# Performance work log

Measured on AMD Instinct MI355X. Metric: run time of the kernel, lower is better.

## Reference

```python
import jax, jax.numpy as jnp
import numpy as np

N_NODES = 100000
N_EDGES = 1600000
DIM = 64
NEG_SLOPE = 0.2  # DGL GATConv default
BN_EPS = 1e-5


def setup_inputs() -> dict:
    key = jax.random.key(0)
    ks = jax.random.split(key, 16)
    d = {}
    d["node_weight"] = jax.random.normal(ks[0], (N_NODES, DIM), jnp.float32)
    d["edge_weight"] = jax.random.normal(ks[1], (N_EDGES,), jnp.float32)  # unused in forward (faithful to source)
    d["src"] = jax.random.randint(ks[2], (N_EDGES,), 0, N_NODES)
    d["dst"] = jax.random.randint(ks[3], (N_EDGES,), 0, N_NODES)
    i = 4
    scale = 1.0 / np.sqrt(DIM)
    for l in (1, 2, 3):
        d[f"W{l}"] = jax.random.normal(ks[i], (DIM, DIM), jnp.float32) * scale; i += 1
        d[f"al{l}"] = jax.random.normal(ks[i], (DIM,), jnp.float32) * 0.1; i += 1
        d[f"ar{l}"] = jax.random.normal(ks[i], (DIM,), jnp.float32) * 0.1; i += 1
        d[f"b{l}"] = jnp.zeros((DIM,), jnp.float32)
        d[f"g{l}"] = jnp.ones((DIM,), jnp.float32)
        d[f"beta{l}"] = jnp.zeros((DIM,), jnp.float32)
    return d


def gat_layer(h, src, dst, W, al, ar, b):
    # DGL GATConv, 1 head: project, edge attention, per-dst softmax, scatter-add
    feat = h @ W                                  # [N, D]
    el = feat @ al                                # [N]
    er = feat @ ar                                # [N]
    e = jax.nn.leaky_relu(el[src] + er[dst], NEG_SLOPE)   # [E]
    m = jax.ops.segment_max(e, dst, num_segments=N_NODES)  # per-dst max
    ex = jnp.exp(e - m[dst])
    s = jax.ops.segment_sum(ex, dst, num_segments=N_NODES)
    alpha = ex / s[dst]                           # edge softmax
    out = jax.ops.segment_sum(alpha[:, None] * feat[src], dst, num_segments=N_NODES)
    return out + b


def batchnorm(h, g, beta):
    # BatchNorm1d in training mode: batch stats, biased variance
    mu = jnp.mean(h, axis=0)
    var = jnp.mean(jnp.square(h - mu), axis=0)
    return (h - mu) * jax.lax.rsqrt(var + BN_EPS) * g + beta


def reference(node_weight, edge_weight, src, dst,
              W1, al1, ar1, b1, g1, beta1,
              W2, al2, ar2, b2, g2, beta2,
              W3, al3, ar3, b3, g3, beta3):
    # dropout is identity in eval mode
    h = gat_layer(node_weight, src, dst, W1, al1, ar1, b1)
    h = jax.nn.elu(batchnorm(h, g1, beta1))
    h = gat_layer(h, src, dst, W2, al2, ar2, b2)
    h = jax.nn.elu(batchnorm(h, g2, beta2))
    h = gat_layer(h, src, dst, W3, al3, ar3, b3)
    h = batchnorm(h, g3, beta3)
    return h
```

## Files before the change

### kernel.cpp

```cpp
#include <hip/hip_runtime.h>
#include <hip/hip_bf16.h>
#include <math.h>

#define DIM 64
#define BSHIFT 9
#define BNODES 512
#define MAXB 256
#define EPT 8
#define CHUNK 2048

typedef __attribute__((ext_vector_type(8))) short bf16x8;
typedef __attribute__((ext_vector_type(4))) float f32x4;

__device__ __forceinline__ short f2bf(float x) {
    union { __hip_bfloat16 b; short s; } u;
    u.b = __float2bfloat16(x);
    return u.s;
}
__device__ __forceinline__ float bf2f(short s) {
    return __uint_as_float(((unsigned)(unsigned short)s) << 16);
}


__global__ void bin_count_kernel(const int* __restrict__ dst, int* __restrict__ bucket_cnt, int E) {
    __shared__ int h[MAXB];
    int t = threadIdx.x;
    h[t] = 0;
    __syncthreads();
    for (int i = blockIdx.x * blockDim.x + t; i < E; i += gridDim.x * blockDim.x)
        atomicAdd(&h[dst[i] >> BSHIFT], 1);
    __syncthreads();
    if (h[t]) atomicAdd(&bucket_cnt[t], h[t]);
}

__global__ void bucket_scan_kernel(const int* __restrict__ bucket_cnt,
                                   int* __restrict__ bucket_off, int* __restrict__ bucket_fill) {
    __shared__ int s[MAXB];
    int t = threadIdx.x;
    int v = bucket_cnt[t];
    s[t] = v;
    __syncthreads();
    for (int off = 1; off < MAXB; off <<= 1) {
        int x = (t >= off) ? s[t - off] : 0;
        __syncthreads();
        s[t] += x;
        __syncthreads();
    }
    bucket_off[t] = s[t] - v;
    bucket_fill[t] = 0;
}

__global__ __launch_bounds__(256) void bin_scatter_kernel(
    const int* __restrict__ src, const int* __restrict__ dst,
    const int* __restrict__ bucket_off, int* __restrict__ bucket_fill,
    unsigned long long* __restrict__ binned, int E) {
    __shared__ int lcnt[MAXB];
    __shared__ int lbase[MAXB];
    int t = threadIdx.x;
    lcnt[t] = 0;
    __syncthreads();
    int base = blockIdx.x * CHUNK;
    unsigned long long pair[EPT];
    int slot[EPT];
#pragma unroll
    for (int j = 0; j < EPT; j++) {
        int idx = base + j * 256 + t;
        if (idx < E) {
            int s = src[idx], d = dst[idx];
            pair[j] = ((unsigned long long)(unsigned)d << 32) | (unsigned)s;
            slot[j] = atomicAdd(&lcnt[d >> BSHIFT], 1);
        } else {
            slot[j] = -1;
        }
    }
    __syncthreads();
    int c = lcnt[t];
    if (c) lbase[t] = atomicAdd(&bucket_fill[t], c);
    __syncthreads();
#pragma unroll
    for (int j = 0; j < EPT; j++) {
        if (slot[j] >= 0) {
            int b = (int)(pair[j] >> 32) >> BSHIFT;
            binned[(size_t)bucket_off[b] + lbase[b] + slot[j]] = pair[j];
        }
    }
}

__global__ __launch_bounds__(256) void node_count_kernel(
    const unsigned long long* __restrict__ binned, const int* __restrict__ bucket_off,
    const int* __restrict__ bucket_cnt, int* __restrict__ counts, int N) {
    __shared__ int cnt[BNODES];
    int b = blockIdx.x, t = threadIdx.x;
    for (int i = t; i < BNODES; i += 256) cnt[i] = 0;
    __syncthreads();
    int s0 = bucket_off[b], c = bucket_cnt[b];
    for (int i = t; i < c; i += 256) {
        int d = (int)(binned[(size_t)s0 + i] >> 32);
        atomicAdd(&cnt[d & (BNODES - 1)], 1);
    }
    __syncthreads();
    int nbase = b << BSHIFT;
    for (int i = t; i < BNODES; i += 256)
        if (nbase + i < N) counts[nbase + i] = cnt[i];
}

__global__ void scan1_kernel(const int* __restrict__ counts, int* __restrict__ excl,
                             int* __restrict__ blk_sums, int n) {
    __shared__ int sdata[256];
    int t = threadIdx.x;
    int base = blockIdx.x * 1024 + t * 4;
    int v0 = (base + 0 < n) ? counts[base + 0] : 0;
    int v1 = (base + 1 < n) ? counts[base + 1] : 0;
    int v2 = (base + 2 < n) ? counts[base + 2] : 0;
    int v3 = (base + 3 < n) ? counts[base + 3] : 0;
    int tsum = v0 + v1 + v2 + v3;
    sdata[t] = tsum;
    __syncthreads();
    for (int off = 1; off < 256; off <<= 1) {
        int x = (t >= off) ? sdata[t - off] : 0;
        __syncthreads();
        sdata[t] += x;
        __syncthreads();
    }
    int run = sdata[t] - tsum;
    if (base + 0 < n) excl[base + 0] = run; run += v0;
    if (base + 1 < n) excl[base + 1] = run; run += v1;
    if (base + 2 < n) excl[base + 2] = run; run += v2;
    if (base + 3 < n) excl[base + 3] = run;
    if (t == 255) blk_sums[blockIdx.x] = sdata[255];
}

__global__ void scan2_kernel(int* __restrict__ blk_sums, int nb) {
    __shared__ int s[128];
    int t = threadIdx.x;
    s[t] = (t < nb) ? blk_sums[t] : 0;
    __syncthreads();
    for (int off = 1; off < 128; off <<= 1) {
        int x = (t >= off) ? s[t - off] : 0;
        __syncthreads();
        s[t] += x;
        __syncthreads();
    }
    if (t < nb) blk_sums[t] = (t > 0) ? s[t - 1] : 0;
}

__global__ void scan3_kernel(int* __restrict__ excl, const int* __restrict__ blk_sums,
                             int n, int total) {
    int i = blockIdx.x * blockDim.x + threadIdx.x;
    if (i < n) excl[i] += blk_sums[i >> 10];
    if (i == 0) excl[n] = total;
}

__global__ __launch_bounds__(256) void final_scatter_kernel(
    const unsigned long long* __restrict__ binned, const int* __restrict__ bucket_off,
    const int* __restrict__ bucket_cnt, const int* __restrict__ row_ptr,
    int* __restrict__ src_sorted, int N) {
    __shared__ int fill[BNODES];
    int b = blockIdx.x, t = threadIdx.x;
    for (int i = t; i < BNODES; i += 256) fill[i] = 0;
    __syncthreads();
    int s0 = bucket_off[b], c = bucket_cnt[b];
    for (int i = t; i < c; i += 256) {
        unsigned long long p = binned[(size_t)s0 + i];
        int d = (int)(p >> 32);
        int pos = row_ptr[d] + atomicAdd(&fill[d & (BNODES - 1)], 1);
        src_sorted[pos] = (int)(p & 0xffffffffu);
    }
}


__global__ __launch_bounds__(256) void gemm64_mfma_kernel(
    const float* __restrict__ h, const float* __restrict__ W,
    const float* __restrict__ al, const float* __restrict__ ar,
    const float* __restrict__ stats, const float* __restrict__ g,
    const float* __restrict__ beta, int do_bn, float invN,
    __hip_bfloat16* __restrict__ feat, float* __restrict__ el, float* __restrict__ er,
    int n) {
    int t = threadIdx.x;
    int lane = t & 63;
    int li = lane & 15;
    int quad = lane >> 4;
    int wv = t >> 6;

    bf16x8 b_hi[2][4], b_lo[2][4];
#pragma unroll
    for (int ks = 0; ks < 2; ks++)
#pragma unroll
        for (int nt = 0; nt < 4; nt++) {
#pragma unroll
            for (int j = 0; j < 8; j++) {
                float w = W[(ks * 32 + quad * 8 + j) * 64 + nt * 16 + li];
                short hi = f2bf(w);
                b_hi[ks][nt][j] = hi;
                b_lo[ks][nt][j] = f2bf(w - bf2f(hi));
            }
        }
    float alv[4], arv[4];
#pragma unroll
    for (int nt = 0; nt < 4; nt++) { alv[nt] = al[nt * 16 + li]; arv[nt] = ar[nt * 16 + li]; }

    float sc[2][8], sh[2][8];
    if (do_bn) {
#pragma unroll
        for (int ks = 0; ks < 2; ks++)
#pragma unroll
            for (int j = 0; j < 8; j++) {
                int k = ks * 32 + quad * 8 + j;
                float mu = stats[k] * invN;
                float var = fmaf(-mu, mu, stats[64 + k] * invN);
                float inv = rsqrtf(var + 1e-5f) * g[k];
                sc[ks][j] = inv;
                sh[ks][j] = beta[k] - mu * inv;
            }
    }

    int ntiles = (n + 15) >> 4;
    for (int tile = blockIdx.x * 4 + wv; tile < ntiles; tile += gridDim.x * 4) {
        int m0 = tile << 4;
        int rrow = m0 + li;
        const float* rowp = h + (size_t)((rrow < n) ? rrow : (n - 1)) * 64;
        bf16x8 a_hi[2], a_lo[2];
#pragma unroll
        for (int ks = 0; ks < 2; ks++) {
            float4 v0 = *(const float4*)(rowp + ks * 32 + quad * 8);
            float4 v1 = *(const float4*)(rowp + ks * 32 + quad * 8 + 4);
            float x[8] = {v0.x, v0.y, v0.z, v0.w, v1.x, v1.y, v1.z, v1.w};
#pragma unroll
            for (int j = 0; j < 8; j++) {
                float v = x[j];
                if (do_bn) {
                    v = fmaf(v, sc[ks][j], sh[ks][j]);
                    if (v < 0.f) v = expm1f(v);
                }
                short hi = f2bf(v);
                a_hi[ks][j] = hi;
                a_lo[ks][j] = f2bf(v - bf2f(hi));
            }
        }
        f32x4 acc[4];
#pragma unroll
        for (int nt = 0; nt < 4; nt++) acc[nt] = (f32x4){0.f, 0.f, 0.f, 0.f};
#pragma unroll
        for (int ks = 0; ks < 2; ks++)
#pragma unroll
            for (int nt = 0; nt < 4; nt++) {
                acc[nt] = __builtin_amdgcn_mfma_f32_16x16x32_bf16(a_hi[ks], b_hi[ks][nt], acc[nt], 0, 0, 0);
                acc[nt] = __builtin_amdgcn_mfma_f32_16x16x32_bf16(a_lo[ks], b_hi[ks][nt], acc[nt], 0, 0, 0);
                acc[nt] = __builtin_amdgcn_mfma_f32_16x16x32_bf16(a_hi[ks], b_lo[ks][nt], acc[nt], 0, 0, 0);
            }
#pragma unroll
        for (int nt = 0; nt < 4; nt++)
#pragma unroll
            for (int reg = 0; reg < 4; reg++) {
                int wrow = m0 + quad * 4 + reg;
                if (wrow < n) {
                    union { __hip_bfloat16 b; short s; } u;
                    u.s = f2bf(acc[nt][reg]);
                    feat[(size_t)wrow * 64 + nt * 16 + li] = u.b;
                }
            }
        float pl[4], pr[4];
#pragma unroll
        for (int reg = 0; reg < 4; reg++) {
            float l = 0.f, r = 0.f;
#pragma unroll
            for (int nt = 0; nt < 4; nt++) {
                l = fmaf(acc[nt][reg], alv[nt], l);
                r = fmaf(acc[nt][reg], arv[nt], r);
            }
#pragma unroll
            for (int off = 1; off < 16; off <<= 1) {
                l += __shfl_xor(l, off, 64);
                r += __shfl_xor(r, off, 64);
            }
            pl[reg] = l; pr[reg] = r;
        }
        int row = m0 + quad * 4;
        if (li == 0 && row < n)          { el[row] = pl[0]; er[row] = pr[0]; }
        else if (li == 1 && row + 1 < n) { el[row + 1] = pl[1]; er[row + 1] = pr[1]; }
        else if (li == 2 && row + 2 < n) { el[row + 2] = pl[2]; er[row + 2] = pr[2]; }
        else if (li == 3 && row + 3 < n) { el[row + 3] = pl[3]; er[row + 3] = pr[3]; }
    }
}

__global__ __launch_bounds__(256) void attn_agg_kernel(
    const int* __restrict__ row_ptr, const int* __restrict__ src_sorted,
    const float* __restrict__ el, const float* __restrict__ er,
    const __hip_bfloat16* __restrict__ feat, const float* __restrict__ bias,
    float* __restrict__ out, int n) {
    int t = threadIdx.x, lane = t & 63;
    int q = lane >> 3;
    int li = lane & 7;
    int node = blockIdx.x * 4 + (t >> 6);
    if (node >= n) return;
    int start = row_ptr[node], end = row_ptr[node + 1];
    float er_n = er[node];
    const uint4* featv = (const uint4*)feat;

    float s = 0.f;
    float a0 = 0.f, a1 = 0.f, a2 = 0.f, a3 = 0.f, a4 = 0.f, a5 = 0.f, a6 = 0.f, a7 = 0.f;

    int i = start;
    bool v0 = false;
    uint4 p0 = {0u, 0u, 0u, 0u};
    float el0 = 0.f;
    if (i < end) {
        int idx = i + q;
        v0 = idx < end;
        int idc = v0 ? idx : end - 1;
        int sn = src_sorted[idc];
        el0 = el[sn];
        p0 = featv[(size_t)sn * 8 + li];
    }
    while (i < end) {
        int inext = i + 8;
        bool v1 = false;
        uint4 p1 = {0u, 0u, 0u, 0u};
        float el1 = 0.f;
        if (inext < end) {
            int idx = inext + q;
            v1 = idx < end;
            int idc = v1 ? idx : end - 1;
            int sn = src_sorted[idc];
            el1 = el[sn];
            p1 = featv[(size_t)sn * 8 + li];
        }
        float e = el0 + er_n;
        e = (e > 0.f) ? e : 0.2f * e;
        float w = v0 ? __expf(e) : 0.f;
        s += w;
        a0 = fmaf(w, __uint_as_float(p0.x << 16), a0);
        a1 = fmaf(w, __uint_as_float(p0.x & 0xffff0000u), a1);
        a2 = fmaf(w, __uint_as_float(p0.y << 16), a2);
        a3 = fmaf(w, __uint_as_float(p0.y & 0xffff0000u), a3);
        a4 = fmaf(w, __uint_as_float(p0.z << 16), a4);
        a5 = fmaf(w, __uint_as_float(p0.z & 0xffff0000u), a5);
        a6 = fmaf(w, __uint_as_float(p0.w << 16), a6);
        a7 = fmaf(w, __uint_as_float(p0.w & 0xffff0000u), a7);
        i = inext; v0 = v1; p0 = p1; el0 = el1;
    }
#pragma unroll
    for (int off = 8; off <= 32; off <<= 1) {
        s  += __shfl_xor(s,  off, 64);
        a0 += __shfl_xor(a0, off, 64);
        a1 += __shfl_xor(a1, off, 64);
        a2 += __shfl_xor(a2, off, 64);
        a3 += __shfl_xor(a3, off, 64);
        a4 += __shfl_xor(a4, off, 64);
        a5 += __shfl_xor(a5, off, 64);
        a6 += __shfl_xor(a6, off, 64);
        a7 += __shfl_xor(a7, off, 64);
    }
    float inv_s = (s > 0.f) ? 1.f / s : 0.f;
    if (q == 0) {
        const float4* bv = (const float4*)bias;
        float4 b0 = bv[li * 2], b1 = bv[li * 2 + 1];
        float4 o0 = {fmaf(a0, inv_s, b0.x), fmaf(a1, inv_s, b0.y),
                     fmaf(a2, inv_s, b0.z), fmaf(a3, inv_s, b0.w)};
        float4 o1 = {fmaf(a4, inv_s, b1.x), fmaf(a5, inv_s, b1.y),
                     fmaf(a6, inv_s, b1.z), fmaf(a7, inv_s, b1.w)};
        float4* op = (float4*)(out + (size_t)node * 64 + li * 8);
        op[0] = o0;
        op[1] = o1;
    }
}

__global__ __launch_bounds__(256) void bn_stats_kernel(const float* __restrict__ h,
                                                       float* __restrict__ stats, int n) {
    __shared__ float ls[256], lss[256];
    int t = threadIdx.x, lane = t & 63;
    int w = blockIdx.x * 4 + (t >> 6);
    int stride = gridDim.x * 4;
    float s = 0.f, ss = 0.f;
    for (int row = w; row < n; row += stride) {
        float v = h[(size_t)row * DIM + lane];
        s += v;
        ss = fmaf(v, v, ss);
    }
    ls[t] = s; lss[t] = ss;
    __syncthreads();
    if (t < 64) {
        float a = ls[t] + ls[t + 64] + ls[t + 128] + ls[t + 192];
        float b = lss[t] + lss[t + 64] + lss[t + 128] + lss[t + 192];
        atomicAdd(&stats[t], a);
        atomicAdd(&stats[64 + t], b);
    }
}

__global__ void bn_apply_kernel(float* __restrict__ h, const float* __restrict__ stats,
                                const float* __restrict__ g, const float* __restrict__ beta,
                                int n, int do_elu) {
    int i = blockIdx.x * blockDim.x + threadIdx.x;
    int total = n * DIM;
    int stride = gridDim.x * blockDim.x;
    float invN = 1.f / (float)n;
    for (; i < total; i += stride) {
        int c = i & 63;
        float mu = stats[c] * invN;
        float var = fmaf(-mu, mu, stats[DIM + c] * invN);
        float x = (h[i] - mu) * rsqrtf(var + 1e-5f) * g[c] + beta[c];
        if (do_elu && x < 0.f) x = expm1f(x);
        h[i] = x;
    }
}


extern "C" void kernel_launch(void* const* d_in, const int* in_sizes, int n_in,
                              void* d_out, int out_size, void* d_ws, size_t ws_size,
                              hipStream_t stream) {
    const float* nw = (const float*)d_in[0];
    const int* src = (const int*)d_in[2];
    const int* dst = (const int*)d_in[3];
    const int N = in_sizes[0] / DIM;
    const int E = in_sizes[2];
    const float invN = 1.f / (float)N;
    const int nbuck = (N + BNODES - 1) >> BSHIFT;

    char* ws = (char*)d_ws;
    size_t off = 0;
    auto alloc = [&](size_t bytes) -> void* {
        void* p = ws + off;
        off += (bytes + 255) & ~(size_t)255;
        return p;
    };
    int* counts       = (int*)alloc((size_t)N * 4);
    int* row_ptr      = (int*)alloc(((size_t)N + 1) * 4);
    int* blk_sums     = (int*)alloc(512);
    int* bucket_cnt   = (int*)alloc(MAXB * 4);
    int* bucket_off   = (int*)alloc(MAXB * 4);
    int* bucket_fill  = (int*)alloc(MAXB * 4);
    unsigned long long* binned = (unsigned long long*)alloc((size_t)E * 8);
    int* src_sorted   = (int*)alloc((size_t)E * 4);
    float* el         = (float*)alloc((size_t)N * 4);
    float* er         = (float*)alloc((size_t)N * 4);
    __hip_bfloat16* feat = (__hip_bfloat16*)alloc((size_t)N * DIM * 2);
    float* hbuf       = (float*)alloc((size_t)N * DIM * 4);
    float* stats      = (float*)alloc(3 * 512);

    int nb = (N + 1023) / 1024;

    hipMemsetAsync(bucket_cnt, 0, MAXB * 4, stream);
    hipMemsetAsync(stats, 0, 3 * 512, stream);
    bin_count_kernel<<<256, 256, 0, stream>>>(dst, bucket_cnt, E);
    bucket_scan_kernel<<<1, MAXB, 0, stream>>>(bucket_cnt, bucket_off, bucket_fill);
    bin_scatter_kernel<<<(E + CHUNK - 1) / CHUNK, 256, 0, stream>>>(
        src, dst, bucket_off, bucket_fill, binned, E);
    node_count_kernel<<<nbuck, 256, 0, stream>>>(binned, bucket_off, bucket_cnt, counts, N);
    scan1_kernel<<<nb, 256, 0, stream>>>(counts, row_ptr, blk_sums, N);
    scan2_kernel<<<1, 128, 0, stream>>>(blk_sums, nb);
    scan3_kernel<<<(N + 255) / 256, 256, 0, stream>>>(row_ptr, blk_sums, N, E);
    final_scatter_kernel<<<nbuck, 256, 0, stream>>>(binned, bucket_off, bucket_cnt,
                                                    row_ptr, src_sorted, N);

    for (int l = 0; l < 3; l++) {
        const float* W    = (const float*)d_in[4 + 6 * l];
        const float* al   = (const float*)d_in[5 + 6 * l];
        const float* ar   = (const float*)d_in[6 + 6 * l];
        const float* b    = (const float*)d_in[7 + 6 * l];
        const float* g    = (const float*)d_in[8 + 6 * l];
        const float* beta = (const float*)d_in[9 + 6 * l];
        const float* hin = (l == 0) ? nw : hbuf;
        float* hout = (l == 2) ? (float*)d_out : hbuf;
        float* stats_prev = stats + (l - 1) * 128;
        float* stats_cur  = stats + l * 128;

        gemm64_mfma_kernel<<<1024, 256, 0, stream>>>(
            hin, W, al, ar, stats_prev,
            (l == 0) ? al : (const float*)d_in[8 + 6 * (l - 1)],
            (l == 0) ? al : (const float*)d_in[9 + 6 * (l - 1)],
            (l > 0) ? 1 : 0, invN,
            feat, el, er, N);
        attn_agg_kernel<<<(N + 3) / 4, 256, 0, stream>>>(row_ptr, src_sorted, el, er,
                                                         feat, b, hout, N);
        bn_stats_kernel<<<512, 256, 0, stream>>>(hout, stats_cur, N);
    }
    bn_apply_kernel<<<2048, 256, 0, stream>>>((float*)d_out, stats + 2 * 128,
                                              (const float*)d_in[8 + 12],
                                              (const float*)d_in[9 + 12],
                                              N, 0);
}
```

Baseline: 469.4 us.

## Fold attention vectors into weights and deepen prefetch in aggregation

Precomputes W·al and W·ar (scaled by log2e) in a tiny kernel so el/er are computed from the input row before the MFMA, replacing the post-GEMM shuffle reduction. The aggregation kernel now prefetches two edge groups ahead, uses exp2 with masked -inf logits, packed FMA accumulation, and a transpose-style cross-lane reduction that writes one scalar output per lane. Together these aim to cut latency stalls and shuffle/ALU work in the gather-dominated aggregation, at the cost of more registers and slightly different rounding of el/er.

```diff
diff --git a/kernel.cpp b/kernel.cpp
--- a/kernel.cpp
+++ b/kernel.cpp
@@ -11,6 +11,7 @@
 
 typedef __attribute__((ext_vector_type(8))) short bf16x8;
 typedef __attribute__((ext_vector_type(4))) float f32x4;
+typedef __attribute__((ext_vector_type(2))) float f32x2;
 
 __device__ __forceinline__ short f2bf(float x) {
     union { __hip_bfloat16 b; short s; } u;
@@ -19,6 +20,15 @@
 }
 __device__ __forceinline__ float bf2f(short s) {
     return __uint_as_float(((unsigned)(unsigned short)s) << 16);
+}
+__device__ __forceinline__ void pk_fma(f32x2& d, f32x2 a, f32x2 b) {
+    asm("v_pk_fma_f32 %0, %1, %2, %0" : "+v"(d) : "v"(a), "v"(b));
+}
+__device__ __forceinline__ f32x2 shfl2(f32x2 v, int mask) {
+    f32x2 r;
+    r.x = __shfl_xor(v.x, mask, 64);
+    r.y = __shfl_xor(v.y, mask, 64);
+    return r;
 }
 
 
@@ -169,9 +179,29 @@
 }
 
 
+__global__ void wlr_kernel(
+    const float* __restrict__ W1, const float* __restrict__ al1, const float* __restrict__ ar1,
+    const float* __restrict__ W2, const float* __restrict__ al2, const float* __restrict__ ar2,
+    const float* __restrict__ W3, const float* __restrict__ al3, const float* __restrict__ ar3,
+    float* __restrict__ wlr) {
+    const float* W  = (blockIdx.x == 0) ? W1  : (blockIdx.x == 1) ? W2  : W3;
+    const float* al = (blockIdx.x == 0) ? al1 : (blockIdx.x == 1) ? al2 : al3;
+    const float* ar = (blockIdx.x == 0) ? ar1 : (blockIdx.x == 1) ? ar2 : ar3;
+    int k = threadIdx.x;
+    float l = 0.f, r = 0.f;
+    for (int nn = 0; nn < 64; nn++) {
+        float w = W[k * 64 + nn];
+        l = fmaf(w, al[nn], l);
+        r = fmaf(w, ar[nn], r);
+    }
+    const float LOG2E = 1.4426950408889634f;
+    wlr[blockIdx.x * 128 + k] = l * LOG2E;
+    wlr[blockIdx.x * 128 + 64 + k] = r * LOG2E;
+}
+
 __global__ __launch_bounds__(256) void gemm64_mfma_kernel(
     const float* __restrict__ h, const float* __restrict__ W,
-    const float* __restrict__ al, const float* __restrict__ ar,
+    const float* __restrict__ wl, const float* __restrict__ wr,
     const float* __restrict__ stats, const float* __restrict__ g,
     const float* __restrict__ beta, int do_bn, float invN,
     __hip_bfloat16* __restrict__ feat, float* __restrict__ el, float* __restrict__ er,
@@ -195,9 +225,14 @@
                 b_lo[ks][nt][j] = f2bf(w - bf2f(hi));
             }
         }
-    float alv[4], arv[4];
-#pragma unroll
-    for (int nt = 0; nt < 4; nt++) { alv[nt] = al[nt * 16 + li]; arv[nt] = ar[nt * 16 + li]; }
+    float wlv[2][8], wrv[2][8];
+#pragma unroll
+    for (int ks = 0; ks < 2; ks++)
+#pragma unroll
+        for (int j = 0; j < 8; j++) {
+            wlv[ks][j] = wl[ks * 32 + quad * 8 + j];
+            wrv[ks][j] = wr[ks * 32 + quad * 8 + j];
+        }
 
     float sc[2][8], sh[2][8];
     if (do_bn) {
@@ -220,6 +255,7 @@
         int rrow = m0 + li;
         const float* rowp = h + (size_t)((rrow < n) ? rrow : (n - 1)) * 64;
         bf16x8 a_hi[2], a_lo[2];
+        float elp = 0.f, erp = 0.f;
 #pragma unroll
         for (int ks = 0; ks < 2; ks++) {
             float4 v0 = *(const float4*)(rowp + ks * 32 + quad * 8);
@@ -232,10 +268,20 @@
                     v = fmaf(v, sc[ks][j], sh[ks][j]);
                     if (v < 0.f) v = expm1f(v);
                 }
+                elp = fmaf(v, wlv[ks][j], elp);
+                erp = fmaf(v, wrv[ks][j], erp);
                 short hi = f2bf(v);
                 a_hi[ks][j] = hi;
                 a_lo[ks][j] = f2bf(v - bf2f(hi));
             }
+        }
+        elp += __shfl_xor(elp, 16, 64);
+        elp += __shfl_xor(elp, 32, 64);
+        erp += __shfl_xor(erp, 16, 64);
+        erp += __shfl_xor(erp, 32, 64);
+        if (lane < 16 && m0 + li < n) {
+            el[m0 + li] = elp;
+            er[m0 + li] = erp;
         }
         f32x4 acc[4];
 #pragma unroll
@@ -259,27 +305,6 @@
                     feat[(size_t)wrow * 64 + nt * 16 + li] = u.b;
                 }
             }
-        float pl[4], pr[4];
-#pragma unroll
-        for (int reg = 0; reg < 4; reg++) {
-            float l = 0.f, r = 0.f;
-#pragma unroll
-            for (int nt = 0; nt < 4; nt++) {
-                l = fmaf(acc[nt][reg], alv[nt], l);
-                r = fmaf(acc[nt][reg], arv[nt], r);
-            }
-#pragma unroll
-            for (int off = 1; off < 16; off <<= 1) {
-                l += __shfl_xor(l, off, 64);
-                r += __shfl_xor(r, off, 64);
-            }
-            pl[reg] = l; pr[reg] = r;
-        }
-        int row = m0 + quad * 4;
-        if (li == 0 && row < n)          { el[row] = pl[0]; er[row] = pr[0]; }
-        else if (li == 1 && row + 1 < n) { el[row + 1] = pl[1]; er[row + 1] = pr[1]; }
-        else if (li == 2 && row + 2 < n) { el[row + 2] = pl[2]; er[row + 2] = pr[2]; }
-        else if (li == 3 && row + 3 < n) { el[row + 3] = pl[3]; er[row + 3] = pr[3]; }
     }
 }
 
@@ -298,71 +323,74 @@
     const uint4* featv = (const uint4*)feat;
 
     float s = 0.f;
-    float a0 = 0.f, a1 = 0.f, a2 = 0.f, a3 = 0.f, a4 = 0.f, a5 = 0.f, a6 = 0.f, a7 = 0.f;
-
-    int i = start;
-    bool v0 = false;
-    uint4 p0 = {0u, 0u, 0u, 0u};
-    float el0 = 0.f;
-    if (i < end) {
-        int idx = i + q;
-        v0 = idx < end;
-        int idc = v0 ? idx : end - 1;
+    f32x2 a01 = {0.f, 0.f}, a23 = {0.f, 0.f}, a45 = {0.f, 0.f}, a67 = {0.f, 0.f};
+
+    uint4 p0 = {0u, 0u, 0u, 0u}, p1 = {0u, 0u, 0u, 0u};
+    float el0 = -INFINITY, el1 = -INFINITY;
+    if (start < end) {
+        int idx = start + q;
+        bool v = idx < end;
+        int idc = v ? idx : end - 1;
         int sn = src_sorted[idc];
-        el0 = el[sn];
+        float ev = el[sn];
+        el0 = v ? ev : -INFINITY;
         p0 = featv[(size_t)sn * 8 + li];
     }
-    while (i < end) {
-        int inext = i + 8;
-        bool v1 = false;
-        uint4 p1 = {0u, 0u, 0u, 0u};
-        float el1 = 0.f;
-        if (inext < end) {
-            int idx = inext + q;
-            v1 = idx < end;
-            int idc = v1 ? idx : end - 1;
+    if (start + 8 < end) {
+        int idx = start + 8 + q;
+        bool v = idx < end;
+        int idc = v ? idx : end - 1;
+        int sn = src_sorted[idc];
+        float ev = el[sn];
+        el1 = v ? ev : -INFINITY;
+        p1 = featv[(size_t)sn * 8 + li];
+    }
+    for (int i = start; i < end; i += 8) {
+        int i2 = i + 16;
+        uint4 p2 = {0u, 0u, 0u, 0u};
+        float el2 = -INFINITY;
+        if (i2 < end) {
+            int idx = i2 + q;
+            bool v = idx < end;
+            int idc = v ? idx : end - 1;
             int sn = src_sorted[idc];
-            el1 = el[sn];
-            p1 = featv[(size_t)sn * 8 + li];
+            float ev = el[sn];
+            el2 = v ? ev : -INFINITY;
+            p2 = featv[(size_t)sn * 8 + li];
         }
         float e = el0 + er_n;
-        e = (e > 0.f) ? e : 0.2f * e;
-        float w = v0 ? __expf(e) : 0.f;
+        e = fmaxf(e, 0.2f * e);
+        float w = exp2f(e);
         s += w;
-        a0 = fmaf(w, __uint_as_float(p0.x << 16), a0);
-        a1 = fmaf(w, __uint_as_float(p0.x & 0xffff0000u), a1);
-        a2 = fmaf(w, __uint_as_float(p0.y << 16), a2);
-        a3 = fmaf(w, __uint_as_float(p0.y & 0xffff0000u), a3);
-        a4 = fmaf(w, __uint_as_float(p0.z << 16), a4);
-        a5 = fmaf(w, __uint_as_float(p0.z & 0xffff0000u), a5);
-        a6 = fmaf(w, __uint_as_float(p0.w << 16), a6);
-        a7 = fmaf(w, __uint_as_float(p0.w & 0xffff0000u), a7);
-        i = inext; v0 = v1; p0 = p1; el0 = el1;
-    }
-#pragma unroll
-    for (int off = 8; off <= 32; off <<= 1) {
-        s  += __shfl_xor(s,  off, 64);
-        a0 += __shfl_xor(a0, off, 64);
-        a1 += __shfl_xor(a1, off, 64);
-        a2 += __shfl_xor(a2, off, 64);
-        a3 += __shfl_xor(a3, off, 64);
-        a4 += __shfl_xor(a4, off, 64);
-        a5 += __shfl_xor(a5, off, 64);
-        a6 += __shfl_xor(a6, off, 64);
-        a7 += __shfl_xor(a7, off, 64);
-    }
+        f32x2 ww = {w, w};
+        f32x2 f;
+        f.x = __uint_as_float(p0.x << 16); f.y = __uint_as_float(p0.x & 0xffff0000u);
+        pk_fma(a01, ww, f);
+        f.x = __uint_as_float(p0.y << 16); f.y = __uint_as_float(p0.y & 0xffff0000u);
+        pk_fma(a23, ww, f);
+        f.x = __uint_as_float(p0.z << 16); f.y = __uint_as_float(p0.z & 0xffff0000u);
+        pk_fma(a45, ww, f);
+        f.x = __uint_as_float(p0.w << 16); f.y = __uint_as_float(p0.w & 0xffff0000u);
+        pk_fma(a67, ww, f);
+        p0 = p1; el0 = el1; p1 = p2; el1 = el2;
+    }
+    s += __shfl_xor(s, 8, 64);
+    s += __shfl_xor(s, 16, 64);
+    s += __shfl_xor(s, 32, 64);
+    f32x2 t01 = shfl2(a01, 8), t23 = shfl2(a23, 8);
+    f32x2 t45 = shfl2(a45, 8), t67 = shfl2(a67, 8);
+    bool b0 = (q & 1) != 0;
+    f32x2 x = b0 ? (a45 + t45) : (a01 + t01);
+    f32x2 y = b0 ? (a67 + t67) : (a23 + t23);
+    f32x2 u = shfl2(x, 16), v2 = shfl2(y, 16);
+    bool b1 = (q & 2) != 0;
+    f32x2 z = b1 ? (y + v2) : (x + u);
+    f32x2 zz = shfl2(z, 32);
+    z = z + zz;
+    float val = ((q & 4) != 0) ? z.y : z.x;
+    int d = li * 8 + ((q & 1) << 2) + (q & 2) + ((q >> 2) & 1);
     float inv_s = (s > 0.f) ? 1.f / s : 0.f;
-    if (q == 0) {
-        const float4* bv = (const float4*)bias;
-        float4 b0 = bv[li * 2], b1 = bv[li * 2 + 1];
-        float4 o0 = {fmaf(a0, inv_s, b0.x), fmaf(a1, inv_s, b0.y),
-                     fmaf(a2, inv_s, b0.z), fmaf(a3, inv_s, b0.w)};
-        float4 o1 = {fmaf(a4, inv_s, b1.x), fmaf(a5, inv_s, b1.y),
-                     fmaf(a6, inv_s, b1.z), fmaf(a7, inv_s, b1.w)};
-        float4* op = (float4*)(out + (size_t)node * 64 + li * 8);
-        op[0] = o0;
-        op[1] = o1;
-    }
+    out[(size_t)node * 64 + d] = fmaf(val, inv_s, bias[d]);
 }
 
 __global__ __launch_bounds__(256) void bn_stats_kernel(const float* __restrict__ h,
@@ -436,11 +464,17 @@
     __hip_bfloat16* feat = (__hip_bfloat16*)alloc((size_t)N * DIM * 2);
     float* hbuf       = (float*)alloc((size_t)N * DIM * 4);
     float* stats      = (float*)alloc(3 * 512);
+    float* wlr        = (float*)alloc(3 * 128 * 4);
 
     int nb = (N + 1023) / 1024;
 
     hipMemsetAsync(bucket_cnt, 0, MAXB * 4, stream);
     hipMemsetAsync(stats, 0, 3 * 512, stream);
+    wlr_kernel<<<3, 64, 0, stream>>>(
+        (const float*)d_in[4],  (const float*)d_in[5],  (const float*)d_in[6],
+        (const float*)d_in[10], (const float*)d_in[11], (const float*)d_in[12],
+        (const float*)d_in[16], (const float*)d_in[17], (const float*)d_in[18],
+        wlr);
     bin_count_kernel<<<256, 256, 0, stream>>>(dst, bucket_cnt, E);
     bucket_scan_kernel<<<1, MAXB, 0, stream>>>(bucket_cnt, bucket_off, bucket_fill);
     bin_scatter_kernel<<<(E + CHUNK - 1) / CHUNK, 256, 0, stream>>>(
@@ -453,21 +487,18 @@
                                                     row_ptr, src_sorted, N);
 
     for (int l = 0; l < 3; l++) {
-        const float* W    = (const float*)d_in[4 + 6 * l];
-        const float* al   = (const float*)d_in[5 + 6 * l];
-        const float* ar   = (const float*)d_in[6 + 6 * l];
         const float* b    = (const float*)d_in[7 + 6 * l];
-        const float* g    = (const float*)d_in[8 + 6 * l];
-        const float* beta = (const float*)d_in[9 + 6 * l];
         const float* hin = (l == 0) ? nw : hbuf;
         float* hout = (l == 2) ? (float*)d_out : hbuf;
-        float* stats_prev = stats + (l - 1) * 128;
+        float* stats_prev = (l == 0) ? stats : stats + (l - 1) * 128;
         float* stats_cur  = stats + l * 128;
 
         gemm64_mfma_kernel<<<1024, 256, 0, stream>>>(
-            hin, W, al, ar, stats_prev,
-            (l == 0) ? al : (const float*)d_in[8 + 6 * (l - 1)],
-            (l == 0) ? al : (const float*)d_in[9 + 6 * (l - 1)],
+            hin, (const float*)d_in[4 + 6 * l],
+            wlr + l * 128, wlr + l * 128 + 64,
+            stats_prev,
+            (l == 0) ? (const float*)d_in[8] : (const float*)d_in[8 + 6 * (l - 1)],
+            (l == 0) ? (const float*)d_in[9] : (const float*)d_in[9 + 6 * (l - 1)],
             (l > 0) ? 1 : 0, invN,
             feat, el, er, N);
         attn_agg_kernel<<<(N + 3) / 4, 256, 0, stream>>>(row_ptr, src_sorted, el, er,
```

Measured after the change: 471.9 us. No clear change (+0.5%).
